# Performance work log

Measured on AMD Instinct MI355X. Metric: run time of the kernel, lower is better.

## Reference

```python
import math
import jax, jax.numpy as jnp
import numpy as np

B, H, T, D = 1, 4, 1024, 8192  # D = 128 * 256 // 4 (hardcoded module constants)
THETA = 2.0 ** 16


def _frequency(d):
    # quantize(arange(d)) = floor(t/2)*2 ; freq = 1/theta**(q/d)/(2*pi)
    t = jnp.arange(d, dtype=jnp.float32)
    q = jnp.floor(t / 2.0) * 2.0
    return 1.0 / (THETA ** (q / d)) / (2.0 * math.pi)  # [D]


def _rope(v):
    # Faithful to original: slices dim 1 (heads), then row-major reshape back.
    v_rot = jnp.stack([-v[:, 1::2], v[:, ::2]], axis=-1).reshape(v.shape)
    freq = _frequency(v.shape[-1])  # [D]
    phases = jnp.arange(v.shape[2], dtype=jnp.float32)[:, None] * freq[None, :]  # [T, D]
    phases = (phases % 1.0) * (2.0 * math.pi)
    cos = jnp.cos(phases)[None, None]  # [1,1,T,D]
    sin = jnp.sin(phases)[None, None]
    return (v * cos).astype(v.dtype) + (v_rot * sin).astype(v.dtype)


def setup_inputs() -> dict:
    key = jax.random.key(0)
    k1, k2 = jax.random.split(key)
    query = jax.random.normal(k1, (B, H, T, D), dtype=jnp.float32)
    value = jax.random.normal(k2, (B, H, T, D), dtype=jnp.float32)
    return {"query": query, "value": value}


def reference(query, value):
    # key is query (asserted in original)
    q = _rope(query)  # [B,H,T,D]
    scale = 1.0 / math.sqrt(D)
    scores = jnp.einsum('bhtd,bhsd->bhts', q, q) * scale  # [B,H,T,T]
    t_idx = jnp.arange(T)
    causal = t_idx[:, None] > t_idx[None, :]  # tril(diagonal=-1): strictly lower
    scores = jnp.where(causal[None, None], scores, 0.0)
    return jnp.einsum('bhts,bhsd->bhtd', scores, value)
```

## Files before the change

### kernel.cpp

```cpp
#include <hip/hip_runtime.h>
#include <hip/hip_bf16.h>


typedef __bf16 bf16x8 __attribute__((ext_vector_type(8)));
typedef float  f32x4  __attribute__((ext_vector_type(4)));

#define HEAD_STRIDE (1024ull * 8192ull)

__device__ inline void gl_lds16(const void* g, void* l) {
  __builtin_amdgcn_global_load_lds(
      (__attribute__((address_space(1))) void*)(g),
      (__attribute__((address_space(3))) void*)(l), 16, 0, 0);
}

__global__ __launch_bounds__(256) void rope_kernel(const float* __restrict__ Q,
                                                   __bf16* __restrict__ Qr) {
  int gid = blockIdx.x * 256 + threadIdx.x;
  size_t e8 = (size_t)gid * 8;
  int d0 = (int)(e8 & 8191);
  int t  = (int)((e8 >> 13) & 1023);
  int h  = (int)(e8 >> 23);

  f32x4 qa = *(const f32x4*)(Q + e8);
  f32x4 qb = *(const f32x4*)(Q + e8 + 4);
  int pt   = t & 1;
  int srct = ((h & 1) << 9) + (t >> 1);
  int sd   = (d0 >> 1) + (pt << 12);
  int hh   = h & ~1;
  size_t soff = ((size_t)srct << 13) + (size_t)sd;
  f32x4 a4 = *(const f32x4*)(Q + (size_t)(hh + 1) * HEAD_STRIDE + soff);
  f32x4 b4 = *(const f32x4*)(Q + (size_t)hh       * HEAD_STRIDE + soff);

  float qv[8];
#pragma unroll
  for (int i = 0; i < 4; ++i) { qv[i] = qa[i]; qv[4 + i] = qb[i]; }

  bf16x8 o;
  float tf = (float)t;
#pragma unroll
  for (int p = 0; p < 4; ++p) {
    float qd = (float)(d0 + 2 * p);
    float fr = exp2f(-qd * (1.0f / 512.0f)) * 0.15915494309189535f;
    float x = tf * fr;
    x -= floorf(x);
    float sn, cs;
    __sincosf(x * 6.283185307179586f, &sn, &cs);
    o[2 * p]     = (__bf16)(qv[2 * p]     * cs - a4[p] * sn);
    o[2 * p + 1] = (__bf16)(qv[2 * p + 1] * cs + b4[p] * sn);
  }
  *(bf16x8*)(Qr + e8) = o;
}

__global__ __launch_bounds__(256) void s1_qqt(const __bf16* __restrict__ Qr,
                                              float* __restrict__ S32) {
  __shared__ __align__(16) __bf16 As[128 * 64];
  __shared__ __align__(16) __bf16 Bs[128 * 64];
  int bid = blockIdx.x;
  int split = bid & 7; bid >>= 3;
  int pair = bid % 36, h = bid / 36;
  int ti = 0, p = pair;
  while (p > ti) { p -= ti + 1; ++ti; }
  int si = p;

  const __bf16* Abase = Qr + (size_t)h * HEAD_STRIDE + ((size_t)(ti * 128) << 13) + split * 1024;
  const __bf16* Bbase = Qr + (size_t)h * HEAD_STRIDE + ((size_t)(si * 128) << 13) + split * 1024;

  int tid = threadIdx.x, lane = tid & 63, wave = tid >> 6;
  int wm = (wave & 1) << 6, wn = (wave >> 1) << 6;
  int l16 = lane & 15, q4 = lane >> 4;
  int srow = lane >> 3;
  int scol = ((lane & 7) ^ srow) * 8;

  f32x4 acc[4][4] = {};

  for (int kk = 0; kk < 1024; kk += 64) {
#pragma unroll
    for (int j = 0; j < 4; ++j) {
      int c = wave * 4 + j;
      int row = c * 8 + srow;
      gl_lds16(Abase + (size_t)row * 8192 + kk + scol, &As[c * 512]);
      gl_lds16(Bbase + (size_t)row * 8192 + kk + scol, &Bs[c * 512]);
    }
    __syncthreads();
#pragma unroll
    for (int ks = 0; ks < 64; ks += 32) {
      bf16x8 af[4], bfr[4];
#pragma unroll
      for (int i = 0; i < 4; ++i) {
        int r = wm + i * 16 + l16;
        af[i] = *(const bf16x8*)&As[r * 64 + (((q4 + (ks >> 3)) ^ (r & 7)) << 3)];
      }
#pragma unroll
      for (int i = 0; i < 4; ++i) {
        int r = wn + i * 16 + l16;
        bfr[i] = *(const bf16x8*)&Bs[r * 64 + (((q4 + (ks >> 3)) ^ (r & 7)) << 3)];
      }
#pragma unroll
      for (int i = 0; i < 4; ++i)
#pragma unroll
        for (int j = 0; j < 4; ++j)
          acc[i][j] = __builtin_amdgcn_mfma_f32_16x16x32_bf16(af[i], bfr[j], acc[i][j], 0, 0, 0);
    }
    __syncthreads();
  }

  const float scale = 0.011048543456039806f;
  int t_base = ti * 128 + wm, s_base = si * 128 + wn;
  float* Sh = S32 + ((size_t)h << 20);
#pragma unroll
  for (int i = 0; i < 4; ++i)
#pragma unroll
    for (int j = 0; j < 4; ++j) {
      int col = s_base + j * 16 + l16;
#pragma unroll
      for (int r = 0; r < 4; ++r) {
        int row = t_base + i * 16 + q4 * 4 + r;
        if (col < row)
          atomicAdd(&Sh[((size_t)row << 10) + col], acc[i][j][r] * scale);
      }
    }
}

__global__ __launch_bounds__(256) void cvt_kernel(const float* __restrict__ S32,
                                                  __bf16* __restrict__ Sbf) {
  int gid = blockIdx.x * 256 + threadIdx.x;
  size_t e = (size_t)gid * 8;
  f32x4 a = *(const f32x4*)(S32 + e);
  f32x4 b = *(const f32x4*)(S32 + e + 4);
  bf16x8 o;
#pragma unroll
  for (int i = 0; i < 4; ++i) { o[i] = (__bf16)a[i]; o[4 + i] = (__bf16)b[i]; }
  *(bf16x8*)(Sbf + e) = o;
}

__global__ __launch_bounds__(256) void transp_kernel(const float* __restrict__ V,
                                                     __bf16* __restrict__ Vt) {
  __shared__ __bf16 L[64 * 72];
  int bid = blockIdx.x;
  int dtile = bid & 127;
  int st = (bid >> 7) & 15;
  int h = bid >> 11;
  int s0 = st << 6, d0 = dtile << 6;
  const float* Vh = V + (size_t)h * HEAD_STRIDE;
  __bf16* Vth = Vt + (size_t)h * HEAD_STRIDE;
  int tid = threadIdx.x;
  int r = tid >> 2;
  int c = (tid & 3) << 4;
#pragma unroll
  for (int j = 0; j < 4; ++j) {
    f32x4 v = *(const f32x4*)(Vh + (size_t)(s0 + r) * 8192 + d0 + c + 4 * j);
#pragma unroll
    for (int e = 0; e < 4; ++e) L[(c + 4 * j + e) * 72 + r] = (__bf16)v[e];
  }
  __syncthreads();
  int row = tid >> 3;
  int col8 = (tid & 7) << 3;
#pragma unroll
  for (int half = 0; half < 2; ++half) {
    int dr = row + half * 32;
    bf16x8 v = *(const bf16x8*)&L[dr * 72 + col8];
    *(bf16x8*)(Vth + (size_t)(d0 + dr) * 1024 + s0 + col8) = v;
  }
}

__global__ __launch_bounds__(256) void s3_sv(const __bf16* __restrict__ Sbf,
                                             const __bf16* __restrict__ Vt,
                                             float* __restrict__ out) {
  __shared__ __align__(16) __bf16 As[128 * 64];
  __shared__ __align__(16) __bf16 Bs[128 * 64];
  int bid = blockIdx.x;
  int dt = bid & 63; bid >>= 6;
  int tt = 7 - (bid & 7);
  int h = bid >> 3;

  const __bf16* Abase = Sbf + ((size_t)h << 20) + ((size_t)(tt * 128) << 10);
  const __bf16* Bbase = Vt + (size_t)h * HEAD_STRIDE + ((size_t)(dt * 128) << 10);
  int Kmax = tt * 128 + 128;

  int tid = threadIdx.x, lane = tid & 63, wave = tid >> 6;
  int wm = (wave & 1) << 6, wn = (wave >> 1) << 6;
  int l16 = lane & 15, q4 = lane >> 4;
  int srow = lane >> 3;
  int scol = ((lane & 7) ^ srow) * 8;

  f32x4 acc[4][4] = {};

  for (int kk = 0; kk < Kmax; kk += 64) {
#pragma unroll
    for (int j = 0; j < 4; ++j) {
      int c = wave * 4 + j;
      int row = c * 8 + srow;
      gl_lds16(Abase + (size_t)row * 1024 + kk + scol, &As[c * 512]);
      gl_lds16(Bbase + (size_t)row * 1024 + kk + scol, &Bs[c * 512]);
    }
    __syncthreads();
#pragma unroll
    for (int ks = 0; ks < 64; ks += 32) {
      bf16x8 af[4], bfr[4];
#pragma unroll
      for (int i = 0; i < 4; ++i) {
        int r = wm + i * 16 + l16;
        af[i] = *(const bf16x8*)&As[r * 64 + (((q4 + (ks >> 3)) ^ (r & 7)) << 3)];
      }
#pragma unroll
      for (int i = 0; i < 4; ++i) {
        int r = wn + i * 16 + l16;
        bfr[i] = *(const bf16x8*)&Bs[r * 64 + (((q4 + (ks >> 3)) ^ (r & 7)) << 3)];
      }
#pragma unroll
      for (int i = 0; i < 4; ++i)
#pragma unroll
        for (int j = 0; j < 4; ++j)
          acc[i][j] = __builtin_amdgcn_mfma_f32_16x16x32_bf16(af[i], bfr[j], acc[i][j], 0, 0, 0);
    }
    __syncthreads();
  }

  int t_base = tt * 128 + wm, d_base = dt * 128 + wn;
  float* obase = out + (size_t)h * HEAD_STRIDE;
#pragma unroll
  for (int i = 0; i < 4; ++i)
#pragma unroll
    for (int j = 0; j < 4; ++j) {
      int col = d_base + j * 16 + l16;
#pragma unroll
      for (int r = 0; r < 4; ++r) {
        int row = t_base + i * 16 + q4 * 4 + r;
        obase[((size_t)row << 13) + col] = acc[i][j][r];
      }
    }
}

extern "C" void kernel_launch(void* const* d_in, const int* in_sizes, int n_in,
                              void* d_out, int out_size, void* d_ws, size_t ws_size,
                              hipStream_t stream) {
  const float* query = (const float*)d_in[0];
  const float* value = (const float*)d_in[1];
  float* out = (float*)d_out;

  char* ws = (char*)d_ws;
  __bf16* Qr  = (__bf16*)ws;
  __bf16* Vt  = (__bf16*)ws;
  float*  S32 = (float*) (ws + 67108864);
  __bf16* Sbf = (__bf16*)(ws + 83886080);

  hipMemsetAsync(S32, 0, 16777216, stream);
  rope_kernel<<<16384, 256, 0, stream>>>(query, Qr);
  s1_qqt<<<1152, 256, 0, stream>>>(Qr, S32);
  transp_kernel<<<8192, 256, 0, stream>>>(value, Vt);
  cvt_kernel<<<2048, 256, 0, stream>>>(S32, Sbf);
  s3_sv<<<2048, 256, 0, stream>>>(Sbf, Vt, out);
}
```

Before: 460.0 us.

## Replace atomic split-K accumulation with bf16 partial buffers and a reduce kernel

The QQ^T stage drops from 8 K-splits to 4. Fp32 atomicAdds into a zeroed S buffer are replaced: split 0 writes its bf16 tile straight into S, and the other splits write bf16 partial tiles to scratch. A new reduce kernel sums the partials, applies the strict causal mask on diagonal tiles and replaces the fp32-to-bf16 convert pass. This removes atomic traffic and shrinks the memset and conversion work, at the cost of halving the grid to 576 blocks, adding partial-buffer traffic, and rounding partial sums to bf16 before they are added.

```diff
diff --git a/kernel.cpp b/kernel.cpp
--- a/kernel.cpp
+++ b/kernel.cpp
@@ -52,18 +52,23 @@
 }
 
 __global__ __launch_bounds__(256) void s1_qqt(const __bf16* __restrict__ Qr,
-                                              float* __restrict__ S32) {
+                                              __bf16* __restrict__ Sbf,
+                                              __bf16* __restrict__ part) {
   __shared__ __align__(16) __bf16 As[128 * 64];
   __shared__ __align__(16) __bf16 Bs[128 * 64];
   int bid = blockIdx.x;
-  int split = bid & 7; bid >>= 3;
-  int pair = bid % 36, h = bid / 36;
+  int x = bid & 7;
+  int g = bid >> 3;
+  int hi = (g >= 36) ? 1 : 0;
+  int pair = g - 36 * hi;
+  int c = x * 2 + hi;
+  int h = c >> 2, split = c & 3;
   int ti = 0, p = pair;
   while (p > ti) { p -= ti + 1; ++ti; }
   int si = p;
 
-  const __bf16* Abase = Qr + (size_t)h * HEAD_STRIDE + ((size_t)(ti * 128) << 13) + split * 1024;
-  const __bf16* Bbase = Qr + (size_t)h * HEAD_STRIDE + ((size_t)(si * 128) << 13) + split * 1024;
+  const __bf16* Abase = Qr + (size_t)h * HEAD_STRIDE + ((size_t)(ti * 128) << 13) + split * 2048;
+  const __bf16* Bbase = Qr + (size_t)h * HEAD_STRIDE + ((size_t)(si * 128) << 13) + split * 2048;
 
   int tid = threadIdx.x, lane = tid & 63, wave = tid >> 6;
   int wm = (wave & 1) << 6, wn = (wave >> 1) << 6;
@@ -73,13 +78,13 @@
 
   f32x4 acc[4][4] = {};
 
-  for (int kk = 0; kk < 1024; kk += 64) {
+  for (int kk = 0; kk < 2048; kk += 64) {
 #pragma unroll
     for (int j = 0; j < 4; ++j) {
-      int c = wave * 4 + j;
-      int row = c * 8 + srow;
-      gl_lds16(Abase + (size_t)row * 8192 + kk + scol, &As[c * 512]);
-      gl_lds16(Bbase + (size_t)row * 8192 + kk + scol, &Bs[c * 512]);
+      int cc = wave * 4 + j;
+      int row = cc * 8 + srow;
+      gl_lds16(Abase + (size_t)row * 8192 + kk + scol, &As[cc * 512]);
+      gl_lds16(Bbase + (size_t)row * 8192 + kk + scol, &Bs[cc * 512]);
     }
     __syncthreads();
 #pragma unroll
@@ -105,32 +110,62 @@
   }
 
   const float scale = 0.011048543456039806f;
-  int t_base = ti * 128 + wm, s_base = si * 128 + wn;
-  float* Sh = S32 + ((size_t)h << 20);
-#pragma unroll
-  for (int i = 0; i < 4; ++i)
-#pragma unroll
-    for (int j = 0; j < 4; ++j) {
-      int col = s_base + j * 16 + l16;
-#pragma unroll
-      for (int r = 0; r < 4; ++r) {
-        int row = t_base + i * 16 + q4 * 4 + r;
-        if (col < row)
-          atomicAdd(&Sh[((size_t)row << 10) + col], acc[i][j][r] * scale);
-      }
-    }
-}
-
-__global__ __launch_bounds__(256) void cvt_kernel(const float* __restrict__ S32,
-                                                  __bf16* __restrict__ Sbf) {
+  if (split == 0) {
+    __bf16* Sh = Sbf + ((size_t)h << 20);
+    int t_base = ti * 128 + wm, s_base = si * 128 + wn;
+#pragma unroll
+    for (int i = 0; i < 4; ++i)
+#pragma unroll
+      for (int j = 0; j < 4; ++j) {
+        int col = s_base + j * 16 + l16;
+#pragma unroll
+        for (int r = 0; r < 4; ++r) {
+          int row = t_base + i * 16 + q4 * 4 + r;
+          Sh[((size_t)row << 10) + col] = (__bf16)(acc[i][j][r] * scale);
+        }
+      }
+  } else {
+    __bf16* P = part + (((size_t)(h * 36 + pair) * 3 + (split - 1)) << 14);
+#pragma unroll
+    for (int i = 0; i < 4; ++i)
+#pragma unroll
+      for (int j = 0; j < 4; ++j) {
+        int lcol = wn + j * 16 + l16;
+#pragma unroll
+        for (int r = 0; r < 4; ++r) {
+          int lrow = wm + i * 16 + q4 * 4 + r;
+          P[lrow * 128 + lcol] = (__bf16)(acc[i][j][r] * scale);
+        }
+      }
+  }
+}
+
+__global__ __launch_bounds__(256) void reduce_kernel(const __bf16* __restrict__ part,
+                                                     __bf16* __restrict__ Sbf) {
   int gid = blockIdx.x * 256 + threadIdx.x;
-  size_t e = (size_t)gid * 8;
-  f32x4 a = *(const f32x4*)(S32 + e);
-  f32x4 b = *(const f32x4*)(S32 + e + 4);
+  int tile = gid >> 11;
+  int e = (gid & 2047) << 3;
+  int row = e >> 7, col = e & 127;
+  int h = tile / 36, pair = tile % 36;
+  int ti = 0, p = pair;
+  while (p > ti) { p -= ti + 1; ++ti; }
+  int si = p;
+
+  size_t soff = ((size_t)h << 20) + ((size_t)(ti * 128 + row) << 10) + si * 128 + col;
+  bf16x8 s0 = *(const bf16x8*)(Sbf + soff);
+  const __bf16* P = part + ((size_t)tile * 3 << 14) + row * 128 + col;
+  bf16x8 p0 = *(const bf16x8*)(P);
+  bf16x8 p1 = *(const bf16x8*)(P + 16384);
+  bf16x8 p2 = *(const bf16x8*)(P + 32768);
+  bool diag = (ti == si);
   bf16x8 o;
 #pragma unroll
-  for (int i = 0; i < 4; ++i) { o[i] = (__bf16)a[i]; o[4 + i] = (__bf16)b[i]; }
-  *(bf16x8*)(Sbf + e) = o;
+  for (int j = 0; j < 8; ++j) {
+    float v = (float)s0[j] + (float)p0[j] + (float)p1[j] + (float)p2[j];
+    if (diag && (col + j >= row)) v = 0.0f;
+    o[j] = (__bf16)v;
+  }
+  *(bf16x8*)(Sbf + soff) = o;
 }
 
 __global__ __launch_bounds__(256) void transp_kernel(const float* __restrict__ V,
@@ -188,10 +223,10 @@
   for (int kk = 0; kk < Kmax; kk += 64) {
 #pragma unroll
     for (int j = 0; j < 4; ++j) {
-      int c = wave * 4 + j;
-      int row = c * 8 + srow;
-      gl_lds16(Abase + (size_t)row * 1024 + kk + scol, &As[c * 512]);
-      gl_lds16(Bbase + (size_t)row * 1024 + kk + scol, &Bs[c * 512]);
+      int cc = wave * 4 + j;
+      int row = cc * 8 + srow;
+      gl_lds16(Abase + (size_t)row * 1024 + kk + scol, &As[cc * 512]);
+      gl_lds16(Bbase + (size_t)row * 1024 + kk + scol, &Bs[cc * 512]);
     }
     __syncthreads();
 #pragma unroll
@@ -239,15 +274,15 @@
   float* out = (float*)d_out;
 
   char* ws = (char*)d_ws;
-  __bf16* Qr  = (__bf16*)ws;
-  __bf16* Vt  = (__bf16*)ws;
-  float*  S32 = (float*) (ws + 67108864);
-  __bf16* Sbf = (__bf16*)(ws + 83886080);
-
-  hipMemsetAsync(S32, 0, 16777216, stream);
+  __bf16* Qr   = (__bf16*)ws;
+  __bf16* Vt   = (__bf16*)ws;
+  __bf16* Sbf  = (__bf16*)(ws + 67108864);
+  __bf16* part = (__bf16*)(ws + 75497472);
+
+  hipMemsetAsync(Sbf, 0, 8388608, stream);
   rope_kernel<<<16384, 256, 0, stream>>>(query, Qr);
-  s1_qqt<<<1152, 256, 0, stream>>>(Qr, S32);
+  s1_qqt<<<576, 256, 0, stream>>>(Qr, Sbf, part);
+  reduce_kernel<<<1152, 256, 0, stream>>>(part, Sbf);
   transp_kernel<<<8192, 256, 0, stream>>>(value, Vt);
-  cvt_kernel<<<2048, 256, 0, stream>>>(S32, Sbf);
   s3_sv<<<2048, 256, 0, stream>>>(Sbf, Vt, out);
 }
```

After: 453.0 us. No clear change (-1.5%).
